# Optimization experiments

Measured on AMD Instinct MI355X. Metric: run time of the kernel, lower is better.

The kernel has to match this reference:

```python
import jax, jax.numpy as jnp
import numpy as np

HID, AA, ESM = 128, 21, 320
D1 = HID + AA + ESM          # 469
N_GRAPHS = 64
BN_EPS = 1e-5


def _lin_params(key, din, dout):
    k1, k2 = jax.random.split(key)
    s = 1.0 / np.sqrt(din)
    W = jax.random.uniform(k1, (din, dout), jnp.float32, -s, s)
    b = jax.random.uniform(k2, (dout,), jnp.float32, -s, s)
    return W, b


def setup_inputs() -> dict:
    key = jax.random.key(0)
    ks = jax.random.split(key, 16)
    N, E = 30000, 480000
    inp = {
        'prot_x': jax.random.normal(ks[0], (N, 6485), jnp.float32),
        'prot_edge_index': jax.random.randint(ks[1], (2, E), 0, N, jnp.int64),
        'prot_batch': jnp.sort(jax.random.randint(ks[2], (N,), 0, N_GRAPHS, jnp.int64)),
    }
    inp['fl1_W'], inp['fl1_b'] = _lin_params(ks[3], 6165 - 21, HID)
    inp['fl2_W'], inp['fl2_b'] = _lin_params(ks[4], AA, AA)
    inp['fl3_W'], inp['fl3_b'] = _lin_params(ks[5], ESM, ESM)
    inp['pdb1_W'], inp['pdb1_b'] = _lin_params(ks[6], D1, D1)
    inp['pdb2_W'], inp['pdb2_b'] = _lin_params(ks[7], D1, 2 * D1)
    inp['af1_W'], inp['af1_b'] = _lin_params(ks[8], D1, D1)
    inp['af2_W'], inp['af2_b'] = _lin_params(ks[9], D1, 2 * D1)
    inp['pdb3_W'], inp['pdb3_b'] = _lin_params(ks[10], 4 * D1, 4 * D1)
    inp['fc1_W'], inp['fc1_b'] = _lin_params(ks[11], 4 * D1, 1024)
    inp['bn_g'] = jnp.ones((1024,), jnp.float32)
    inp['bn_b'] = jnp.zeros((1024,), jnp.float32)
    inp['fc2_W'], inp['fc2_b'] = _lin_params(ks[12], 1024, 486)
    return inp


def _gcn_graph(edge_index, n):
    # add self-loops, symmetric normalization D^-1/2 (A+I) D^-1/2
    loops = jnp.arange(n, dtype=edge_index.dtype)
    src = jnp.concatenate([edge_index[0], loops])
    dst = jnp.concatenate([edge_index[1], loops])
    deg = jax.ops.segment_sum(jnp.ones_like(dst, jnp.float32), dst, n)
    dinv = jax.lax.rsqrt(jnp.maximum(deg, 1.0))  # deg >= 1 via self-loop
    norm = dinv[src] * dinv[dst]
    return src, dst, norm


def _gcn_conv(x, W, b, src, dst, norm, n):
    h = x @ W                                   # [N, Dout]
    msg = h[src] * norm[:, None]                # gather + scale
    return jax.ops.segment_sum(msg, dst, n) + b  # scatter-add


def reference(prot_x, prot_edge_index, prot_batch,
              fl1_W, fl1_b, fl2_W, fl2_b, fl3_W, fl3_b,
              pdb1_W, pdb1_b, pdb2_W, pdb2_b,
              af1_W, af1_b, af2_W, af2_b,
              pdb3_W, pdb3_b, fc1_W, fc1_b, bn_g, bn_b, fc2_W, fc2_b):
    n = prot_x.shape[0]
    relu = jax.nn.relu
    f1 = relu(prot_x[:, 21:6165] @ fl1_W + fl1_b)   # [N,128]
    f2 = relu(prot_x[:, :21] @ fl2_W + fl2_b)       # [N,21]
    f3 = relu(prot_x[:, 6165:] @ fl3_W + fl3_b)     # [N,320]
    feat = jnp.concatenate([f2, f1, f3], axis=1)    # [N,469]

    src, dst, norm = _gcn_graph(prot_edge_index, n)
    x = relu(_gcn_conv(feat, pdb1_W, pdb1_b, src, dst, norm, n))
    x = relu(_gcn_conv(x, pdb2_W, pdb2_b, src, dst, norm, n))
    y = relu(_gcn_conv(feat, af1_W, af1_b, src, dst, norm, n))
    y = relu(_gcn_conv(y, af2_W, af2_b, src, dst, norm, n))
    z = jnp.concatenate([x, y], axis=1)             # [N, 4*469]
    z = relu(_gcn_conv(z, pdb3_W, pdb3_b, src, dst, norm, n))

    # gap: global mean pool per graph
    cnt = jax.ops.segment_sum(jnp.ones((n,), jnp.float32), prot_batch, N_GRAPHS)
    z = jax.ops.segment_sum(z, prot_batch, N_GRAPHS) / jnp.maximum(cnt, 1.0)[:, None]

    z = z @ fc1_W + fc1_b                            # [G,1024]
    mu = jnp.mean(z, axis=0)
    var = jnp.mean((z - mu) ** 2, axis=0)            # biased, torch BN training math
    z = (z - mu) * jax.lax.rsqrt(var + BN_EPS) * bn_g + bn_b
    z = relu(z)                                      # dropout = identity (eval)
    z = z @ fc2_W + fc2_b
    return jax.nn.sigmoid(z)
```

## Files before the change

kernel.cpp:

```cpp
#include <hip/hip_runtime.h>
#include <hip/hip_bf16.h>
#include <stdint.h>

#define NG 64

typedef __attribute__((ext_vector_type(8))) short bf16x8;
typedef __attribute__((ext_vector_type(4))) float f32x4;

#define AS1 __attribute__((address_space(1)))
#define AS3 __attribute__((address_space(3)))

static __device__ __forceinline__ unsigned short f2b(float f) {
    unsigned u = __float_as_uint(f);
    return (unsigned short)((u + 0x7fffu + ((u >> 16) & 1u)) >> 16);
}
static __device__ __forceinline__ float b2f(unsigned short h) {
    return __uint_as_float(((unsigned)h) << 16);
}
static __device__ __forceinline__ void gl16(const void* g, void* l) {
    __builtin_amdgcn_global_load_lds(
        (const AS1 void*)(uintptr_t)g,
        (AS3 void*)(unsigned)(uintptr_t)l, 16, 0, 0);
}

__global__ void initcnt_k(int* cnt, int n) {
    int i = blockIdx.x * blockDim.x + threadIdx.x;
    if (i < n) cnt[i] = 0;
}
__global__ void count_k(const int* __restrict__ dst, int* cnt, int E) {
    int e = blockIdx.x * blockDim.x + threadIdx.x;
    if (e < E) atomicAdd(&cnt[dst[e]], 1);
}
__global__ void dinv_k(const int* __restrict__ cnt, float* dinv, int n) {
    int i = blockIdx.x * blockDim.x + threadIdx.x;
    if (i < n) dinv[i] = rsqrtf((float)(cnt[i] + 1));
}
__global__ void scan1_k(const int* __restrict__ cnt, int* __restrict__ scan,
                        int* __restrict__ bsum, int n) {
    __shared__ int wsum[16];
    int tid = threadIdx.x, lane = tid & 63, wid = tid >> 6;
    int i = blockIdx.x * 1024 + tid;
    int x = (i < n) ? cnt[i] : 0;
#pragma unroll
    for (int off = 1; off < 64; off <<= 1) {
        int t = __shfl_up(x, off);
        if (lane >= off) x += t;
    }
    if (lane == 63) wsum[wid] = x;
    __syncthreads();
    if (tid < 16) {
        int s = wsum[tid];
#pragma unroll
        for (int off = 1; off < 16; off <<= 1) {
            int t = __shfl_up(s, off);
            if (tid >= off) s += t;
        }
        wsum[tid] = s;
    }
    __syncthreads();
    int add = wid ? wsum[wid - 1] : 0;
    if (i < n) scan[i] = x + add;
    if (tid == 1023) bsum[blockIdx.x] = x + add;
}
__global__ void scan2_k(int* bsum, int nb) {
    int tid = threadIdx.x;
    int x = (tid < nb) ? bsum[tid] : 0;
#pragma unroll
    for (int off = 1; off < 64; off <<= 1) {
        int t = __shfl_up(x, off);
        if (tid >= off) x += t;
    }
    if (tid < nb) bsum[tid] = x;
}
__global__ void scan3_k(const int* __restrict__ scan, const int* __restrict__ bsum,
                        int* __restrict__ rowptr, int n) {
    int i = blockIdx.x * blockDim.x + threadIdx.x;
    if (i == 0) rowptr[0] = 0;
    if (i < n) {
        int b = i >> 10;
        rowptr[i + 1] = scan[i] + (b ? bsum[b - 1] : 0);
    }
}
__global__ void fillinit_k(const int* __restrict__ rowptr, int* fill, int n) {
    int i = blockIdx.x * blockDim.x + threadIdx.x;
    if (i < n) fill[i] = rowptr[i];
}
__global__ void fill_k(const int* __restrict__ src, const int* __restrict__ dst,
                       int* fill, int* csr, int E) {
    int e = blockIdx.x * blockDim.x + threadIdx.x;
    if (e < E) {
        int d = dst[e];
        int pos = atomicAdd(&fill[d], 1);
        csr[pos] = src[e];
    }
}

__global__ void wtconv_k(const float* __restrict__ W, int K, int Nout,
                         unsigned short* __restrict__ Wt, int Kpad, int Nrows, int remap) {
    __shared__ float t[32][33];
    int k0 = blockIdx.x * 32, n0 = blockIdx.y * 32;
    int cx = threadIdx.x & 31, ry = threadIdx.x >> 5;
#pragma unroll
    for (int p = 0; p < 4; ++p) {
        int k = k0 + ry + p * 8, nn = n0 + cx;
        int ko = k;
        bool kvalid;
        if (remap) {
            ko = (k < 448) ? k + 21 : k - 448;
            kvalid = (k < 469);
        } else {
            kvalid = (k < K);
        }
        t[ry + p * 8][cx] = (kvalid && nn < Nout) ? W[(size_t)ko * Nout + nn] : 0.0f;
    }
    __syncthreads();
#pragma unroll
    for (int p = 0; p < 4; ++p) {
        int nn = n0 + ry + p * 8, k = k0 + cx;
        if (nn < Nrows) Wt[(size_t)nn * Kpad + k] = f2b(t[cx][ry + p * 8]);
    }
}

__global__ void biascat_k(const float* __restrict__ b0, const float* __restrict__ b1,
                          float* __restrict__ out) {
    int i = threadIdx.x + blockIdx.x * blockDim.x;
    if (i >= 960) return;
    int seg = i >= 480, c = i - seg * 480;
    const float* b = seg ? b1 : b0;
    out[i] = (c < 469) ? b[c] : 0.0f;
}

__global__ void fl2_k(const float* __restrict__ x, int ldx,
                      const float* __restrict__ W, const float* __restrict__ b,
                      unsigned short* __restrict__ out, int ldo, int n) {
    __shared__ float Ws[441];
    __shared__ float Bs[21];
    int tid = threadIdx.x;
    for (int i = tid; i < 441; i += 256) Ws[i] = W[i];
    if (tid < 21) Bs[tid] = b[tid];
    __syncthreads();
    int row = blockIdx.x * 256 + tid;
    if (row >= n) return;
    float xv[21];
#pragma unroll
    for (int j = 0; j < 21; ++j) xv[j] = x[(size_t)row * ldx + j];
    for (int c = 0; c < 32; ++c) {
        float v = 0.0f;
        if (c < 21) {
            float a = Bs[c];
#pragma unroll
            for (int j = 0; j < 21; ++j) a = fmaf(xv[j], Ws[j * 21 + c], a);
            v = fmaxf(a, 0.0f);
        }
        out[(size_t)row * ldo + 448 + c] = f2b(v);
    }
}

template<bool A32>
__global__ __launch_bounds__(256) void mgemm_t(
    const void* __restrict__ Aptr, int lda, int Mreal,
    const unsigned short* __restrict__ Bt, int ldb,
    const float* __restrict__ bias,
    unsigned short* __restrict__ C, int ldc, int coff,
    int K, int Nout, int Nzero, int GX) {
    __shared__ unsigned short As[128 * 32];
    __shared__ unsigned short Bs[128 * 32];
    const int tid = threadIdx.x;
    const int w = tid >> 6, lane = tid & 63;

    const int nwg = gridDim.x;
    const int q = nwg >> 3, r = nwg & 7;
    const int xcd = blockIdx.x & 7, oidx = blockIdx.x >> 3;
    const int swz = (xcd < r ? xcd * (q + 1) : r * (q + 1) + (xcd - r) * q) + oidx;
    const int m0 = (swz / GX) * 128, n0 = (swz % GX) * 128;

    const int wr = w >> 1, wc = w & 1;

    f32x4 acc[4][4];
#pragma unroll
    for (int i = 0; i < 4; ++i)
#pragma unroll
        for (int j = 0; j < 4; ++j) acc[i][j] = (f32x4){0.f, 0.f, 0.f, 0.f};

    const int ko = (lane >> 4) * 8;
    const int rA = wr * 64 + (lane & 15);
    const int rB = wc * 64 + (lane & 15);

    for (int k0 = 0; k0 < K; k0 += 32) {
        if constexpr (A32) {
            const float* Af = (const float*)Aptr;
#pragma unroll
            for (int j = 0; j < 2; ++j) {
                int c = w * 2 + j;
                int id2 = c * 64 + lane;
                int row = id2 >> 2, cc = id2 & 3;
                int gm = m0 + row; if (gm > Mreal - 1) gm = Mreal - 1;
                const float* ap = Af + (size_t)gm * lda + k0 + cc * 8;
                float4 v0 = *(const float4*)ap;
                float4 v1 = *(const float4*)(ap + 4);
                unsigned short t[8] = {f2b(v0.x), f2b(v0.y), f2b(v0.z), f2b(v0.w),
                                       f2b(v1.x), f2b(v1.y), f2b(v1.z), f2b(v1.w)};
                *(bf16x8*)&As[row * 32 + cc * 8] = *(const bf16x8*)t;
            }
        } else {
            const unsigned short* Ab = (const unsigned short*)Aptr;
#pragma unroll
            for (int j = 0; j < 2; ++j) {
                int c = w * 2 + j;
                int id2 = c * 64 + lane;
                int row = id2 >> 2, cc = id2 & 3;
                gl16(Ab + (size_t)(m0 + row) * lda + k0 + cc * 8, &As[c * 512]);
            }
        }
#pragma unroll
        for (int j = 0; j < 2; ++j) {
            int c = w * 2 + j;
            int id2 = c * 64 + lane;
            int row = id2 >> 2, cc = id2 & 3;
            gl16(Bt + (size_t)(n0 + row) * ldb + k0 + cc * 8, &Bs[c * 512]);
        }
        __syncthreads();
        bf16x8 a[4], b[4];
#pragma unroll
        for (int i = 0; i < 4; ++i) a[i] = *(const bf16x8*)&As[(rA + i * 16) * 32 + ko];
#pragma unroll
        for (int j = 0; j < 4; ++j) b[j] = *(const bf16x8*)&Bs[(rB + j * 16) * 32 + ko];
#pragma unroll
        for (int i = 0; i < 4; ++i)
#pragma unroll
            for (int j = 0; j < 4; ++j)
                acc[i][j] = __builtin_amdgcn_mfma_f32_16x16x32_bf16(a[i], b[j], acc[i][j], 0, 0, 0);
        __syncthreads();
    }

    const int cn = lane & 15, r4 = (lane >> 4) * 4;
    for (int ni = 0; ni < 4; ++ni) {
        int col = n0 + wc * 64 + ni * 16 + cn;
        if (col >= Nzero) continue;
        bool real = col < Nout;
        float bb = real ? bias[col] : 0.0f;
#pragma unroll
        for (int mi = 0; mi < 4; ++mi) {
#pragma unroll
            for (int rr = 0; rr < 4; ++rr) {
                int row = m0 + wr * 64 + mi * 16 + r4 + rr;
                float x = real ? fmaxf(acc[mi][ni][rr] + bb, 0.0f) : 0.0f;
                C[(size_t)row * ldc + coff + col] = f2b(x);
            }
        }
    }
}

__global__ __launch_bounds__(256) void fl1part_k(
    const float* __restrict__ A, int lda, int Mreal,
    const unsigned short* __restrict__ Bt, int ldb,
    float* __restrict__ part, int MT, int Mpad) {
    __shared__ unsigned short As[128 * 32];
    __shared__ unsigned short Bs[128 * 32];
    const int tid = threadIdx.x;
    const int w = tid >> 6, lane = tid & 63;
    const int mt = blockIdx.x % MT, ks = blockIdx.x / MT;
    const int m0 = mt * 128;
    const int kbeg = ks * 2048, kend = kbeg + 2048;
    const int wr = w >> 1, wc = w & 1;

    f32x4 acc[4][4];
#pragma unroll
    for (int i = 0; i < 4; ++i)
#pragma unroll
        for (int j = 0; j < 4; ++j) acc[i][j] = (f32x4){0.f, 0.f, 0.f, 0.f};

    const int ko = (lane >> 4) * 8;
    const int rA = wr * 64 + (lane & 15);
    const int rB = wc * 64 + (lane & 15);

    for (int k0 = kbeg; k0 < kend; k0 += 32) {
#pragma unroll
        for (int j = 0; j < 2; ++j) {
            int c = w * 2 + j;
            int id2 = c * 64 + lane;
            int row = id2 >> 2, cc = id2 & 3;
            int gm = m0 + row; if (gm > Mreal - 1) gm = Mreal - 1;
            const float* ap = A + (size_t)gm * lda + k0 + cc * 8;
            float4 v0 = *(const float4*)ap;
            float4 v1 = *(const float4*)(ap + 4);
            unsigned short t[8] = {f2b(v0.x), f2b(v0.y), f2b(v0.z), f2b(v0.w),
                                   f2b(v1.x), f2b(v1.y), f2b(v1.z), f2b(v1.w)};
            *(bf16x8*)&As[row * 32 + cc * 8] = *(const bf16x8*)t;
            gl16(Bt + (size_t)row * ldb + k0 + cc * 8, &Bs[c * 512]);
        }
        __syncthreads();
        bf16x8 a[4], b[4];
#pragma unroll
        for (int i = 0; i < 4; ++i) a[i] = *(const bf16x8*)&As[(rA + i * 16) * 32 + ko];
#pragma unroll
        for (int j = 0; j < 4; ++j) b[j] = *(const bf16x8*)&Bs[(rB + j * 16) * 32 + ko];
#pragma unroll
        for (int i = 0; i < 4; ++i)
#pragma unroll
            for (int j = 0; j < 4; ++j)
                acc[i][j] = __builtin_amdgcn_mfma_f32_16x16x32_bf16(a[i], b[j], acc[i][j], 0, 0, 0);
        __syncthreads();
    }

    float* pb = part + (size_t)ks * Mpad * 128;
    const int cn = lane & 15, r4 = (lane >> 4) * 4;
#pragma unroll
    for (int ni = 0; ni < 4; ++ni) {
        int col = wc * 64 + ni * 16 + cn;
#pragma unroll
        for (int mi = 0; mi < 4; ++mi) {
#pragma unroll
            for (int rr = 0; rr < 4; ++rr) {
                int row = m0 + wr * 64 + mi * 16 + r4 + rr;
                pb[(size_t)row * 128 + col] = acc[mi][ni][rr];
            }
        }
    }
}

__global__ void fl1red_k(const float* __restrict__ part, const float* __restrict__ bias,
                         unsigned short* __restrict__ feat, int Mpad) {
    int i = blockIdx.x * blockDim.x + threadIdx.x;
    if (i >= Mpad * 32) return;
    int row = i >> 5, c = (i & 31) * 4;
    size_t base = (size_t)row * 128 + c;
    size_t stride = (size_t)Mpad * 128;
    float4 p0 = *(const float4*)(part + base);
    float4 p1 = *(const float4*)(part + stride + base);
    float4 p2 = *(const float4*)(part + 2 * stride + base);
    float4 bb = *(const float4*)(bias + c);
    ushort4 o;
    o.x = f2b(fmaxf(p0.x + p1.x + p2.x + bb.x, 0.0f));
    o.y = f2b(fmaxf(p0.y + p1.y + p2.y + bb.y, 0.0f));
    o.z = f2b(fmaxf(p0.z + p1.z + p2.z + bb.z, 0.0f));
    o.w = f2b(fmaxf(p0.w + p1.w + p2.w + bb.w, 0.0f));
    *(ushort4*)(feat + (size_t)row * 480 + c) = o;
}

__global__ __launch_bounds__(256) void agg_wave_k(
    const unsigned short* __restrict__ in, unsigned short* __restrict__ out,
    const float* __restrict__ dinv, const int* __restrict__ rowptr,
    const int* __restrict__ csr, int D8, int ld, int n) {
    int lane = threadIdx.x & 63;
    int node = blockIdx.x * 4 + (threadIdx.x >> 6);
    if (node >= n) return;
    bool act = lane < D8;
    float di = dinv[node];
    float acc[8];
#pragma unroll
    for (int t = 0; t < 8; ++t) acc[t] = 0.0f;
    if (act) {
        bf16x8 v = *(const bf16x8*)(in + (size_t)node * ld + lane * 8);
#pragma unroll
        for (int t = 0; t < 8; ++t) acc[t] = di * b2f((unsigned short)v[t]);
    }
    int s = rowptr[node], e = rowptr[node + 1];
    for (int c = s; c < e; c += 64) {
        int m = e - c; if (m > 64) m = 64;
        int idx = (c + lane < e) ? csr[c + lane] : 0;
        float wl = dinv[idx];
        for (int j = 0; j < m; ++j) {
            int src = __shfl(idx, j);
            float wgt = __shfl(wl, j);
            if (act) {
                bf16x8 v = *(const bf16x8*)(in + (size_t)src * ld + lane * 8);
#pragma unroll
                for (int t = 0; t < 8; ++t) acc[t] = fmaf(wgt, b2f((unsigned short)v[t]), acc[t]);
            }
        }
    }
    if (act) {
        unsigned short o[8];
#pragma unroll
        for (int t = 0; t < 8; ++t) o[t] = f2b(di * acc[t]);
        *(bf16x8*)(out + (size_t)node * ld + lane * 8) = *(const bf16x8*)o;
    }
}

__global__ void agg_block_k(
    const unsigned short* __restrict__ in, unsigned short* __restrict__ out,
    const float* __restrict__ dinv, const int* __restrict__ rowptr,
    const int* __restrict__ csr, int D8, int ld, int n) {
    int i = blockIdx.x;
    int tid = threadIdx.x;
    __shared__ int s_src[64];
    __shared__ float s_w[64];
    bool act = tid < D8;
    float di = dinv[i];
    float acc[8];
#pragma unroll
    for (int t = 0; t < 8; ++t) acc[t] = 0.0f;
    if (act) {
        bf16x8 v = *(const bf16x8*)(in + (size_t)i * ld + tid * 8);
#pragma unroll
        for (int t = 0; t < 8; ++t) acc[t] = di * b2f((unsigned short)v[t]);
    }
    int s = rowptr[i], e = rowptr[i + 1];
    for (int c = s; c < e; c += 64) {
        int k = c + tid;
        if (tid < 64 && k < e) { int sn = csr[k]; s_src[tid] = sn; s_w[tid] = dinv[sn]; }
        __syncthreads();
        int m = e - c; if (m > 64) m = 64;
        for (int j = 0; j < m; ++j) {
            int sn = s_src[j];
            float wgt = s_w[j];
            if (act) {
                bf16x8 v = *(const bf16x8*)(in + (size_t)sn * ld + tid * 8);
#pragma unroll
                for (int t = 0; t < 8; ++t) acc[t] = fmaf(wgt, b2f((unsigned short)v[t]), acc[t]);
            }
        }
        __syncthreads();
    }
    if (act) {
        unsigned short o[8];
#pragma unroll
        for (int t = 0; t < 8; ++t) o[t] = f2b(di * acc[t]);
        *(bf16x8*)(out + (size_t)i * ld + tid * 8) = *(const bf16x8*)o;
    }
}

__global__ void pool_k(const unsigned short* __restrict__ in, int ld,
                       const int* __restrict__ batch,
                       float* __restrict__ out, int n, int D) {
    int g = blockIdx.y;
    int d8 = blockIdx.x * blockDim.x + threadIdx.x;
    if (d8 * 8 >= ld) return;
    int lo = 0, hi = n;
    while (lo < hi) { int mid = (lo + hi) >> 1; if (batch[mid] < g) lo = mid + 1; else hi = mid; }
    int start = lo;
    lo = start; hi = n;
    while (lo < hi) { int mid = (lo + hi) >> 1; if (batch[mid] < g + 1) lo = mid + 1; else hi = mid; }
    int end = lo;
    float s[8];
#pragma unroll
    for (int j = 0; j < 8; ++j) s[j] = 0.0f;
    for (int r = start; r < end; r++) {
        bf16x8 v = *(const bf16x8*)(in + (size_t)r * ld + d8 * 8);
#pragma unroll
        for (int j = 0; j < 8; ++j) s[j] += b2f((unsigned short)v[j]);
    }
    float inv = 1.0f / fmaxf((float)(end - start), 1.0f);
#pragma unroll
    for (int j = 0; j < 8; ++j) {
        int d = d8 * 8 + j;
        if (d < D) out[(size_t)g * D + d] = s[j] * inv;
    }
}

__global__ __launch_bounds__(256) void sgemm_part_k(
    const float* __restrict__ A, int lda,
    const float* __restrict__ W, int ldw,
    float* __restrict__ part, int K, int Nout, int ksplit) {
    const int n0 = blockIdx.x * 64;
    const int ks = blockIdx.y;
    const int kbeg = (int)(((long long)K * ks) / ksplit);
    const int kend = (int)(((long long)K * (ks + 1)) / ksplit);
    const int tx = threadIdx.x & 63, ty = threadIdx.x >> 6;
    __shared__ float As[64][65];
    float acc[16];
#pragma unroll
    for (int r = 0; r < 16; ++r) acc[r] = 0.0f;

    for (int kb = kbeg; kb < kend; kb += 64) {
        int kc = kend - kb; if (kc > 64) kc = 64;
        for (int i = threadIdx.x; i < 64 * 64; i += 256) {
            int r = i >> 6, c = i & 63;
            As[r][c] = (c < kc) ? A[(size_t)r * lda + kb + c] : 0.0f;
        }
        __syncthreads();
        if (n0 + tx < Nout) {
            for (int k = 0; k < kc; ++k) {
                float w = W[(size_t)(kb + k) * ldw + n0 + tx];
#pragma unroll
                for (int r = 0; r < 16; ++r)
                    acc[r] = fmaf(As[ty * 16 + r][k], w, acc[r]);
            }
        }
        __syncthreads();
    }
    if (n0 + tx < Nout) {
#pragma unroll
        for (int r = 0; r < 16; ++r)
            part[((size_t)ks * 64 + ty * 16 + r) * Nout + n0 + tx] = acc[r];
    }
}

__global__ void sgemm_reduce_k(const float* __restrict__ part, const float* __restrict__ bias,
                               float* __restrict__ C, int ldc, int Nout, int ksplit, int act) {
    int i = blockIdx.x * blockDim.x + threadIdx.x;
    if (i >= NG * Nout) return;
    int m = i / Nout, n = i - m * Nout;
    float v = bias[n];
    for (int s = 0; s < ksplit; ++s) v += part[((size_t)s * 64 + m) * Nout + n];
    if (act == 2) v = 1.0f / (1.0f + expf(-v));
    C[(size_t)m * ldc + n] = v;
}

__global__ void bn_k(const float* __restrict__ z, const float* __restrict__ g,
                     const float* __restrict__ b, float* __restrict__ out) {
    int c = blockIdx.x * blockDim.x + threadIdx.x;
    if (c >= 1024) return;
    float s = 0.0f, s2 = 0.0f;
    for (int r = 0; r < NG; r++) { float v = z[r * 1024 + c]; s += v; s2 += v * v; }
    float mu = s / (float)NG;
    float var = s2 / (float)NG - mu * mu;
    float sc = g[c] * rsqrtf(var + 1e-5f);
    float sh = b[c] - mu * sc;
    for (int r = 0; r < NG; r++)
        out[r * 1024 + c] = fmaxf(fmaf(z[r * 1024 + c], sc, sh), 0.0f);
}

extern "C" void kernel_launch(void* const* d_in, const int* in_sizes, int n_in,
                              void* d_out, int out_size, void* d_ws, size_t ws_size,
                              hipStream_t stream) {
    (void)n_in; (void)out_size; (void)ws_size;
    const float* prot_x = (const float*)d_in[0];
    const int*   eidx   = (const int*)d_in[1];
    const int*   batch  = (const int*)d_in[2];
    const float* fl1_W = (const float*)d_in[3],  *fl1_b = (const float*)d_in[4];
    const float* fl2_W = (const float*)d_in[5],  *fl2_b = (const float*)d_in[6];
    const float* fl3_W = (const float*)d_in[7],  *fl3_b = (const float*)d_in[8];
    const float* pdb1_W = (const float*)d_in[9],  *pdb1_b = (const float*)d_in[10];
    const float* pdb2_W = (const float*)d_in[11], *pdb2_b = (const float*)d_in[12];
    const float* af1_W  = (const float*)d_in[13], *af1_b  = (const float*)d_in[14];
    const float* af2_W  = (const float*)d_in[15], *af2_b  = (const float*)d_in[16];
    const float* pdb3_W = (const float*)d_in[17], *pdb3_b = (const float*)d_in[18];
    const float* fc1_W  = (const float*)d_in[19], *fc1_b  = (const float*)d_in[20];
    const float* bn_g   = (const float*)d_in[21], *bn_b   = (const float*)d_in[22];
    const float* fc2_W  = (const float*)d_in[23], *fc2_b  = (const float*)d_in[24];

    const int N = in_sizes[2];
    const int E = in_sizes[1] / 2;
    const int* e_src = eidx;
    const int* e_dst = eidx + E;
    const int Mpad = ((N + 127) / 128) * 128;
    const int MT = Mpad / 128;
    const int NB = (N + 1023) / 1024;

    char* wp = (char*)d_ws;
    auto alloc = [&](size_t bytes) -> char* {
        char* r = wp; wp += (bytes + 255) & ~(size_t)255; return r;
    };
    unsigned short* feat = (unsigned short*)alloc((size_t)Mpad * 480 * 2);
    unsigned short* tmp1 = (unsigned short*)alloc((size_t)Mpad * 480 * 2);
    unsigned short* hxy  = (unsigned short*)alloc((size_t)Mpad * 960 * 2);
    unsigned short* tmp2 = (unsigned short*)alloc((size_t)Mpad * 960 * 2);
    unsigned short* zb   = (unsigned short*)alloc((size_t)Mpad * 1920 * 2);
    unsigned short* zagg = (unsigned short*)alloc((size_t)Mpad * 1920 * 2);
    unsigned short* zout = (unsigned short*)alloc((size_t)Mpad * 1888 * 2);
    unsigned short* wt_fl1  = (unsigned short*)alloc((size_t)128 * 6144 * 2);
    unsigned short* wt_fl3  = (unsigned short*)alloc((size_t)384 * 320 * 2);
    unsigned short* wt_c1   = (unsigned short*)alloc((size_t)1024 * 480 * 2);
    unsigned short* wt_pdb2 = (unsigned short*)alloc((size_t)1024 * 480 * 2);
    unsigned short* wt_af2  = (unsigned short*)alloc((size_t)1024 * 480 * 2);
    unsigned short* wt_pdb3 = (unsigned short*)alloc((size_t)1920 * 1920 * 2);
    float* f_bias1 = (float*)alloc(960 * 4);
    float* f_dinv = (float*)alloc((size_t)N * 4);
    float* f_pool = (float*)alloc((size_t)NG * 1876 * 4);
    float* f_fc1  = (float*)alloc((size_t)NG * 1024 * 4);
    float* f_bn   = (float*)alloc((size_t)NG * 1024 * 4);
    float* f_part = (float*)alloc((size_t)16 * 64 * 1024 * 4);
    float* f_flp  = (float*)alloc((size_t)3 * Mpad * 128 * 4);
    int* i_cnt    = (int*)alloc((size_t)N * 4);
    int* i_scan   = (int*)alloc((size_t)N * 4);
    int* i_bsum   = (int*)alloc(64 * 4);
    int* i_rowptr = (int*)alloc((size_t)(N + 1) * 4);
    int* i_fill   = (int*)alloc((size_t)N * 4);
    int* i_csr    = (int*)alloc((size_t)E * 4);

    auto mg = [&](const unsigned short* A, int lda, const unsigned short* Wt, int ldb,
                  const float* bias, unsigned short* C, int ldc, int coff,
                  int K, int Nout, int Nzero) {
        int gx = (Nzero + 127) / 128;
        mgemm_t<false><<<gx * MT, 256, 0, stream>>>(
            A, lda, Mpad, Wt, ldb, bias, C, ldc, coff, K, Nout, Nzero, gx);
    };
    auto mgf = [&](const float* A, int lda, const unsigned short* Wt, int ldb,
                   const float* bias, unsigned short* C, int ldc, int coff,
                   int K, int Nout, int Nzero) {
        int gx = (Nzero + 127) / 128;
        mgemm_t<true><<<gx * MT, 256, 0, stream>>>(
            A, lda, N, Wt, ldb, bias, C, ldc, coff, K, Nout, Nzero, gx);
    };
    auto wt = [&](const float* W, int K, int Nout, unsigned short* Wt, int Kpad, int Nrows, int remap) {
        wtconv_k<<<dim3(Kpad / 32, Nrows / 32), 256, 0, stream>>>(W, K, Nout, Wt, Kpad, Nrows, remap);
    };

    initcnt_k<<<(N + 255) / 256, 256, 0, stream>>>(i_cnt, N);
    count_k<<<(E + 255) / 256, 256, 0, stream>>>(e_dst, i_cnt, E);
    dinv_k<<<(N + 255) / 256, 256, 0, stream>>>(i_cnt, f_dinv, N);
    scan1_k<<<NB, 1024, 0, stream>>>(i_cnt, i_scan, i_bsum, N);
    scan2_k<<<1, 64, 0, stream>>>(i_bsum, NB);
    scan3_k<<<(N + 255) / 256, 256, 0, stream>>>(i_scan, i_bsum, i_rowptr, N);
    fillinit_k<<<(N + 255) / 256, 256, 0, stream>>>(i_rowptr, i_fill, N);
    fill_k<<<(E + 255) / 256, 256, 0, stream>>>(e_src, e_dst, i_fill, i_csr, E);

    wt(fl1_W, 6144, 128, wt_fl1, 6144, 128, 0);
    wt(fl3_W, 320, 320, wt_fl3, 320, 384, 0);
    wt(pdb1_W, 469, 469, wt_c1, 480, 480, 1);
    wt(af1_W, 469, 469, wt_c1 + (size_t)480 * 480, 480, 544, 1);
    wt(pdb2_W, 469, 938, wt_pdb2, 480, 1024, 0);
    wt(af2_W, 469, 938, wt_af2, 480, 1024, 0);
    wt(pdb3_W, 1876, 1876, wt_pdb3, 1920, 1920, 0);
    biascat_k<<<4, 256, 0, stream>>>(pdb1_b, af1_b, f_bias1);

    fl2_k<<<(N + 255) / 256, 256, 0, stream>>>(prot_x, 6485, fl2_W, fl2_b, feat, 480, N);
    fl1part_k<<<MT * 3, 256, 0, stream>>>(prot_x + 21, 6485, N, wt_fl1, 6144, f_flp, MT, Mpad);
    fl1red_k<<<(Mpad * 32 + 255) / 256, 256, 0, stream>>>(f_flp, fl1_b, feat, Mpad);
    mgf(prot_x + 6165, 6485, wt_fl3, 320, fl3_b, feat, 480, 128, 320, 320, 320);

    agg_wave_k<<<(N + 3) / 4, 256, 0, stream>>>(feat, tmp1, f_dinv, i_rowptr, i_csr, 60, 480, N);
    mg(tmp1, 480, wt_c1, 480, f_bias1, hxy, 960, 0, 480, 960, 960);
    agg_block_k<<<N, 128, 0, stream>>>(hxy, tmp2, f_dinv, i_rowptr, i_csr, 120, 960, N);
    mg(tmp2,       960, wt_pdb2, 480, pdb2_b, zb, 1920, 0,   480, 938, 938);
    mg(tmp2 + 480, 960, wt_af2,  480, af2_b,  zb, 1920, 938, 480, 938, 982);
    agg_block_k<<<N, 256, 0, stream>>>(zb, zagg, f_dinv, i_rowptr, i_csr, 240, 1920, N);
    mg(zagg, 1920, wt_pdb3, 1920, pdb3_b, zout, 1888, 0, 1920, 1876, 1888);

    pool_k<<<dim3(2, NG), 128, 0, stream>>>(zout, 1888, batch, f_pool, N, 1876);
    sgemm_part_k<<<dim3(16, 16), 256, 0, stream>>>(f_pool, 1876, fc1_W, 1024, f_part, 1876, 1024, 16);
    sgemm_reduce_k<<<(NG * 1024 + 255) / 256, 256, 0, stream>>>(f_part, fc1_b, f_fc1, 1024, 1024, 16, 0);
    bn_k<<<4, 256, 0, stream>>>(f_fc1, bn_g, bn_b, f_bn);
    sgemm_part_k<<<dim3(8, 16), 256, 0, stream>>>(f_bn, 1024, fc2_W, 486, f_part, 1024, 486, 16);
    sgemm_reduce_k<<<(NG * 486 + 255) / 256, 256, 0, stream>>>(f_part, fc2_b, (float*)d_out, 486, 486, 16, 2);
}
```

Baseline: 1.673 ms.

## Widen bf16 GEMM N-tile to 192, fuse CSR setup kernels, retune pooling

The bf16 MFMA GEMM is templated on the N-tile width, and the bf16-input path now uses 128x192 tiles so each A tile is reused across more output columns. The af2 weight buffer is padded to 1152 rows to cover the wider tiles. The dinv, scan3 and fill-init kernels are merged into a single launch to cut launch overhead. The pooling kernel launch shape changes and a row-loop unroll pragma is added. The wider tile raises accumulator register use and can waste work on padded columns.

```diff
diff --git a/kernel.cpp b/kernel.cpp
--- a/kernel.cpp
+++ b/kernel.cpp
@@ -30,10 +30,6 @@
 __global__ void count_k(const int* __restrict__ dst, int* cnt, int E) {
     int e = blockIdx.x * blockDim.x + threadIdx.x;
     if (e < E) atomicAdd(&cnt[dst[e]], 1);
-}
-__global__ void dinv_k(const int* __restrict__ cnt, float* dinv, int n) {
-    int i = blockIdx.x * blockDim.x + threadIdx.x;
-    if (i < n) dinv[i] = rsqrtf((float)(cnt[i] + 1));
 }
 __global__ void scan1_k(const int* __restrict__ cnt, int* __restrict__ scan,
                         int* __restrict__ bsum, int n) {
@@ -72,18 +68,19 @@
     }
     if (tid < nb) bsum[tid] = x;
 }
-__global__ void scan3_k(const int* __restrict__ scan, const int* __restrict__ bsum,
-                        int* __restrict__ rowptr, int n) {
+__global__ void scan3f_k(const int* __restrict__ scan, const int* __restrict__ bsum,
+                         const int* __restrict__ cnt,
+                         int* __restrict__ rowptr, int* __restrict__ fill,
+                         float* __restrict__ dinv, int n) {
     int i = blockIdx.x * blockDim.x + threadIdx.x;
+    if (i >= n) return;
+    int b = i >> 10;
+    int rp1 = scan[i] + (b ? bsum[b - 1] : 0);
+    rowptr[i + 1] = rp1;
+    int rp0 = rp1 - cnt[i];
     if (i == 0) rowptr[0] = 0;
-    if (i < n) {
-        int b = i >> 10;
-        rowptr[i + 1] = scan[i] + (b ? bsum[b - 1] : 0);
-    }
-}
-__global__ void fillinit_k(const int* __restrict__ rowptr, int* fill, int n) {
-    int i = blockIdx.x * blockDim.x + threadIdx.x;
-    if (i < n) fill[i] = rowptr[i];
+    fill[i] = rp0;
+    dinv[i] = rsqrtf((float)(cnt[i] + 1));
 }
 __global__ void fill_k(const int* __restrict__ src, const int* __restrict__ dst,
                        int* fill, int* csr, int E) {
@@ -156,15 +153,16 @@
     }
 }
 
-template<bool A32>
+template<int NI, bool A32>
 __global__ __launch_bounds__(256) void mgemm_t(
     const void* __restrict__ Aptr, int lda, int Mreal,
     const unsigned short* __restrict__ Bt, int ldb,
     const float* __restrict__ bias,
     unsigned short* __restrict__ C, int ldc, int coff,
     int K, int Nout, int Nzero, int GX) {
+    constexpr int BNT = NI * 32;
     __shared__ unsigned short As[128 * 32];
-    __shared__ unsigned short Bs[128 * 32];
+    __shared__ unsigned short Bs[BNT * 32];
     const int tid = threadIdx.x;
     const int w = tid >> 6, lane = tid & 63;
 
@@ -172,19 +170,19 @@
     const int q = nwg >> 3, r = nwg & 7;
     const int xcd = blockIdx.x & 7, oidx = blockIdx.x >> 3;
     const int swz = (xcd < r ? xcd * (q + 1) : r * (q + 1) + (xcd - r) * q) + oidx;
-    const int m0 = (swz / GX) * 128, n0 = (swz % GX) * 128;
+    const int m0 = (swz / GX) * 128, n0 = (swz % GX) * BNT;
 
     const int wr = w >> 1, wc = w & 1;
 
-    f32x4 acc[4][4];
+    f32x4 acc[4][NI];
 #pragma unroll
     for (int i = 0; i < 4; ++i)
 #pragma unroll
-        for (int j = 0; j < 4; ++j) acc[i][j] = (f32x4){0.f, 0.f, 0.f, 0.f};
+        for (int j = 0; j < NI; ++j) acc[i][j] = (f32x4){0.f, 0.f, 0.f, 0.f};
 
     const int ko = (lane >> 4) * 8;
     const int rA = wr * 64 + (lane & 15);
-    const int rB = wc * 64 + (lane & 15);
+    const int rB = wc * (NI * 16) + (lane & 15);
 
     for (int k0 = 0; k0 < K; k0 += 32) {
         if constexpr (A32) {
@@ -213,29 +211,29 @@
             }
         }
 #pragma unroll
-        for (int j = 0; j < 2; ++j) {
-            int c = w * 2 + j;
+        for (int j = 0; j < NI / 2; ++j) {
+            int c = w * (NI / 2) + j;
             int id2 = c * 64 + lane;
             int row = id2 >> 2, cc = id2 & 3;
             gl16(Bt + (size_t)(n0 + row) * ldb + k0 + cc * 8, &Bs[c * 512]);
         }
         __syncthreads();
-        bf16x8 a[4], b[4];
+        bf16x8 a[4], b[NI];
 #pragma unroll
         for (int i = 0; i < 4; ++i) a[i] = *(const bf16x8*)&As[(rA + i * 16) * 32 + ko];
 #pragma unroll
-        for (int j = 0; j < 4; ++j) b[j] = *(const bf16x8*)&Bs[(rB + j * 16) * 32 + ko];
+        for (int j = 0; j < NI; ++j) b[j] = *(const bf16x8*)&Bs[(rB + j * 16) * 32 + ko];
 #pragma unroll
         for (int i = 0; i < 4; ++i)
 #pragma unroll
-            for (int j = 0; j < 4; ++j)
+            for (int j = 0; j < NI; ++j)
                 acc[i][j] = __builtin_amdgcn_mfma_f32_16x16x32_bf16(a[i], b[j], acc[i][j], 0, 0, 0);
         __syncthreads();
     }
 
     const int cn = lane & 15, r4 = (lane >> 4) * 4;
-    for (int ni = 0; ni < 4; ++ni) {
-        int col = n0 + wc * 64 + ni * 16 + cn;
+    for (int ni = 0; ni < NI; ++ni) {
+        int col = n0 + wc * (NI * 16) + ni * 16 + cn;
         if (col >= Nzero) continue;
         bool real = col < Nout;
         float bb = real ? bias[col] : 0.0f;
@@ -436,6 +434,7 @@
     float s[8];
 #pragma unroll
     for (int j = 0; j < 8; ++j) s[j] = 0.0f;
+#pragma unroll 4
     for (int r = start; r < end; r++) {
         bf16x8 v = *(const bf16x8*)(in + (size_t)r * ld + d8 * 8);
 #pragma unroll
@@ -554,7 +553,7 @@
     unsigned short* wt_fl3  = (unsigned short*)alloc((size_t)384 * 320 * 2);
     unsigned short* wt_c1   = (unsigned short*)alloc((size_t)1024 * 480 * 2);
     unsigned short* wt_pdb2 = (unsigned short*)alloc((size_t)1024 * 480 * 2);
-    unsigned short* wt_af2  = (unsigned short*)alloc((size_t)1024 * 480 * 2);
+    unsigned short* wt_af2  = (unsigned short*)alloc((size_t)1152 * 480 * 2);
     unsigned short* wt_pdb3 = (unsigned short*)alloc((size_t)1920 * 1920 * 2);
     float* f_bias1 = (float*)alloc(960 * 4);
     float* f_dinv = (float*)alloc((size_t)N * 4);
@@ -573,15 +572,15 @@
     auto mg = [&](const unsigned short* A, int lda, const unsigned short* Wt, int ldb,
                   const float* bias, unsigned short* C, int ldc, int coff,
                   int K, int Nout, int Nzero) {
-        int gx = (Nzero + 127) / 128;
-        mgemm_t<false><<<gx * MT, 256, 0, stream>>>(
+        int gx = (Nzero + 191) / 192;
+        mgemm_t<6, false><<<gx * MT, 256, 0, stream>>>(
             A, lda, Mpad, Wt, ldb, bias, C, ldc, coff, K, Nout, Nzero, gx);
     };
     auto mgf = [&](const float* A, int lda, const unsigned short* Wt, int ldb,
                    const float* bias, unsigned short* C, int ldc, int coff,
                    int K, int Nout, int Nzero) {
         int gx = (Nzero + 127) / 128;
-        mgemm_t<true><<<gx * MT, 256, 0, stream>>>(
+        mgemm_t<4, true><<<gx * MT, 256, 0, stream>>>(
             A, lda, N, Wt, ldb, bias, C, ldc, coff, K, Nout, Nzero, gx);
     };
     auto wt = [&](const float* W, int K, int Nout, unsigned short* Wt, int Kpad, int Nrows, int remap) {
@@ -590,11 +589,9 @@
 
     initcnt_k<<<(N + 255) / 256, 256, 0, stream>>>(i_cnt, N);
     count_k<<<(E + 255) / 256, 256, 0, stream>>>(e_dst, i_cnt, E);
-    dinv_k<<<(N + 255) / 256, 256, 0, stream>>>(i_cnt, f_dinv, N);
     scan1_k<<<NB, 1024, 0, stream>>>(i_cnt, i_scan, i_bsum, N);
     scan2_k<<<1, 64, 0, stream>>>(i_bsum, NB);
-    scan3_k<<<(N + 255) / 256, 256, 0, stream>>>(i_scan, i_bsum, i_rowptr, N);
-    fillinit_k<<<(N + 255) / 256, 256, 0, stream>>>(i_rowptr, i_fill, N);
+    scan3f_k<<<(N + 255) / 256, 256, 0, stream>>>(i_scan, i_bsum, i_cnt, i_rowptr, i_fill, f_dinv, N);
     fill_k<<<(E + 255) / 256, 256, 0, stream>>>(e_src, e_dst, i_fill, i_csr, E);
 
     wt(fl1_W, 6144, 128, wt_fl1, 6144, 128, 0);
@@ -602,7 +599,7 @@
     wt(pdb1_W, 469, 469, wt_c1, 480, 480, 1);
     wt(af1_W, 469, 469, wt_c1 + (size_t)480 * 480, 480, 544, 1);
     wt(pdb2_W, 469, 938, wt_pdb2, 480, 1024, 0);
-    wt(af2_W, 469, 938, wt_af2, 480, 1024, 0);
+    wt(af2_W, 469, 938, wt_af2, 480, 1152, 0);
     wt(pdb3_W, 1876, 1876, wt_pdb3, 1920, 1920, 0);
     biascat_k<<<4, 256, 0, stream>>>(pdb1_b, af1_b, f_bias1);
 
@@ -619,7 +616,7 @@
     agg_block_k<<<N, 256, 0, stream>>>(zb, zagg, f_dinv, i_rowptr, i_csr, 240, 1920, N);
     mg(zagg, 1920, wt_pdb3, 1920, pdb3_b, zout, 1888, 0, 1920, 1876, 1888);
 
-    pool_k<<<dim3(2, NG), 128, 0, stream>>>(zout, 1888, batch, f_pool, N, 1876);
+    pool_k<<<dim3(4, NG), 64, 0, stream>>>(zout, 1888, batch, f_pool, N, 1876);
     sgemm_part_k<<<dim3(16, 16), 256, 0, stream>>>(f_pool, 1876, fc1_W, 1024, f_part, 1876, 1024, 16);
     sgemm_reduce_k<<<(NG * 1024 + 255) / 256, 256, 0, stream>>>(f_part, fc1_b, f_fc1, 1024, 1024, 16, 0);
     bn_k<<<4, 256, 0, stream>>>(f_fc1, bn_g, bn_b, f_bn);
```

Result: faster. 1.574 ms (-5.9%).
